# Performance work log

Measured on AMD Instinct MI355X. Metric: run time of the kernel, lower is better.

The kernel has to match this reference:

```python
import jax, jax.numpy as jnp
import numpy as np

N, E, IN_DIM, HID, HEADS, LAYERS, NTYPES, NGRAPH = 50000, 600000, 64, 128, 8, 3, 10, 500
C = HID // HEADS
NEG_SLOPE = 0.2
EPS = 1e-5


def setup_inputs() -> dict:
    key = jax.random.key(0)
    ks = jax.random.split(key, 24)
    inp = {
        "x": jax.random.normal(ks[0], (N, IN_DIM), jnp.float32),
        "edge_index": jax.random.randint(ks[1], (2, E), 0, N),
        "node_types": jax.random.randint(ks[2], (N,), 0, NTYPES),
        "batch": jnp.sort(jax.random.randint(ks[3], (N,), 0, NGRAPH)),
        # node embedding linear
        "emb_W": jax.random.normal(ks[4], (IN_DIM, HID), jnp.float32) / np.sqrt(IN_DIM),
        "emb_b": jnp.zeros((HID,), jnp.float32),
        "ntype_emb": jax.random.normal(ks[5], (NTYPES, HID), jnp.float32) * 0.02,
        # stacked GAT layer params
        "gat_W": jax.random.normal(ks[6], (LAYERS, HID, HID), jnp.float32) / np.sqrt(HID),
        "att_src": jax.random.normal(ks[7], (LAYERS, HEADS, C), jnp.float32) * 0.1,
        "att_dst": jax.random.normal(ks[8], (LAYERS, HEADS, C), jnp.float32) * 0.1,
        "gat_b": jnp.zeros((LAYERS, HID), jnp.float32),
        "ln_g": jnp.ones((LAYERS, HID), jnp.float32),
        "ln_b": jnp.zeros((LAYERS, HID), jnp.float32),
        # global attention MLP
        "ga_W1": jax.random.normal(ks[9], (HID, HID), jnp.float32) / np.sqrt(HID),
        "ga_b1": jnp.zeros((HID,), jnp.float32),
        "ga_W2": jax.random.normal(ks[10], (HID, 1), jnp.float32) / np.sqrt(HID),
        "ga_b2": jnp.zeros((1,), jnp.float32),
        # graph classifier head
        "cls_W1": jax.random.normal(ks[11], (HID, HID), jnp.float32) / np.sqrt(HID),
        "cls_b1": jnp.zeros((HID,), jnp.float32),
        "cls_W2": jax.random.normal(ks[12], (HID, 1), jnp.float32) / np.sqrt(HID),
        "cls_b2": jnp.zeros((1,), jnp.float32),
    }
    return inp


def _layer_norm(h, g, b):
    mu = jnp.mean(h, axis=-1, keepdims=True)
    var = jnp.mean(jnp.square(h - mu), axis=-1, keepdims=True)
    return (h - mu) * jax.lax.rsqrt(var + EPS) * g + b


def _gat_layer(h, src, dst, W, a_src, a_dst, bias):
    # h: [N, HID] -> per-head projection [N, H, C]
    hp = (h @ W).reshape(N, HEADS, C)
    alpha_s = jnp.sum(hp * a_src, axis=-1)  # [N, H]
    alpha_d = jnp.sum(hp * a_dst, axis=-1)  # [N, H]
    e = jax.nn.leaky_relu(alpha_s[src] + alpha_d[dst], NEG_SLOPE)  # [E', H]
    # segment softmax over incoming edges of each destination node
    m = jax.ops.segment_max(e, dst, num_segments=N)
    ex = jnp.exp(e - m[dst])
    s = jax.ops.segment_sum(ex, dst, num_segments=N)
    alpha = ex / s[dst]  # every node has a self-loop, so s > 0
    msg = hp[src] * alpha[:, :, None]  # [E', H, C]
    out = jax.ops.segment_sum(msg, dst, num_segments=N)  # [N, H, C]
    return out.reshape(N, HID) + bias


def reference(x, edge_index, node_types, batch, emb_W, emb_b, ntype_emb,
              gat_W, att_src, att_dst, gat_b, ln_g, ln_b,
              ga_W1, ga_b1, ga_W2, ga_b2, cls_W1, cls_b1, cls_W2, cls_b2):
    # self-loops (PyG GATConv add_self_loops=True)
    loop = jnp.arange(N)
    src = jnp.concatenate([edge_index[0], loop])
    dst = jnp.concatenate([edge_index[1], loop])

    h = x @ emb_W + emb_b
    h = h + ntype_emb[node_types]

    for l in range(LAYERS):
        h_prev = h
        h = _gat_layer(h, src, dst, gat_W[l], att_src[l], att_dst[l], gat_b[l])
        h = _layer_norm(h, ln_g[l], ln_b[l])
        h = jax.nn.relu(h + h_prev)

    # global attention pooling: softmax over all nodes (dim 0, as in source)
    scores = jnp.tanh(h @ ga_W1 + ga_b1) @ ga_W2 + ga_b2  # [N, 1]
    attw = jax.nn.softmax(scores, axis=0)
    h_graph = jnp.sum(h * attw, axis=0)  # [HID]

    # global mean pool per graph
    sums = jax.ops.segment_sum(h, batch, num_segments=NGRAPH)  # [G, HID]
    cnts = jax.ops.segment_sum(jnp.ones((N, 1), h.dtype), batch, num_segments=NGRAPH)
    mean_pool = sums / jnp.maximum(cnts, 1.0)

    hg = h_graph + mean_pool  # broadcast [HID] + [G, HID]

    # graph classifier head (features_batch=None path), squeeze(-1)
    out = jax.nn.relu(hg @ cls_W1 + cls_b1) @ cls_W2 + cls_b2
    return out.squeeze(-1)  # [G]
```

## Files before the change

### kernel.cpp

```cpp
#include <hip/hip_runtime.h>
#include <hip/hip_bf16.h>
#include <math.h>

#define HID 128
#define HEADS 8
#define INDIM 64

typedef _Float16 f16x8 __attribute__((ext_vector_type(8)));
typedef _Float16 f16x4 __attribute__((ext_vector_type(4)));
typedef _Float16 f16x2 __attribute__((ext_vector_type(2)));
typedef float f32x4 __attribute__((ext_vector_type(4)));

__device__ __forceinline__ float fast_tanh(float x) {
    return 1.f - 2.f / (__expf(2.f * x) + 1.f);
}

#if defined(__has_builtin)
#if __has_builtin(__builtin_amdgcn_fdot2)
#define HAVE_FDOT2 1
#endif
#endif

__global__ void prologue_kernel(const int* __restrict__ ei, int* __restrict__ deg,
                                const float* __restrict__ emb_W, const float* __restrict__ gat_W,
                                const float* __restrict__ ga_W1, _Float16* __restrict__ wt_emb,
                                _Float16* __restrict__ wt_gat, _Float16* __restrict__ wt_ga1,
                                const int* __restrict__ batch, int* __restrict__ gstart,
                                float* __restrict__ hgZ,
                                int E, int EE, int N, int G) {
    int i = blockIdx.x * blockDim.x + threadIdx.x;
    if (i < EE) {
        int dst = (i < E) ? ei[E + i] : (i - E);
        atomicAdd(&deg[dst], 1);
    }
    if (i < 8192) {
        int k = i >> 7, n = i & 127;
        wt_emb[n * 64 + k] = (_Float16)emb_W[i];
    } else if (i < 8192 + 49152) {
        int j = i - 8192;
        int l = j >> 14, r = j & 16383;
        int k = r >> 7, n = r & 127;
        wt_gat[l * 16384 + n * 128 + k] = (_Float16)gat_W[j];
    } else if (i < 73728) {
        int j = i - 57344;
        int k = j >> 7, n = j & 127;
        wt_ga1[n * 128 + k] = (_Float16)ga_W1[j];
    } else if (i < 73728 + 129) {
        hgZ[i - 73728] = 0.f;
    }
    if (i >= 100000 && i - 100000 <= G) {
        int g = i - 100000;
        int lo = 0, hi = N;
        while (lo < hi) {
            int mid = (lo + hi) >> 1;
            if (batch[mid] < g) lo = mid + 1; else hi = mid;
        }
        gstart[g] = lo;
    }
}

__global__ __launch_bounds__(256) void mfma_proj_kernel(
    int mode, int K, int N,
    const _Float16* __restrict__ A16, const float* __restrict__ Af32,
    const _Float16* __restrict__ Wt,
    const float* __restrict__ bias, const float* __restrict__ nemb,
    const int* __restrict__ ntypes, _Float16* __restrict__ h16out,
    const float* __restrict__ asrc, const float* __restrict__ adst,
    _Float16* __restrict__ hp_out, float* __restrict__ als, float* __restrict__ ald,
    const float* __restrict__ w2, const float* __restrict__ b2,
    float* __restrict__ escore,
    int PB, int task, const int* __restrict__ ei2,
    const int* __restrict__ degc,
    int* __restrict__ rowptrw, int* __restrict__ woffw, int* __restrict__ esrcw,
    int E2, int EE2)
{
    __shared__ _Float16 w_lds[128 * 136];
    __shared__ _Float16 a_lds[64 * 136];
    int t = threadIdx.x;

    if ((int)blockIdx.x >= PB) {
        if (task == 1) {
            int b = (int)blockIdx.x - PB;
            int i = b * 256 + t;
            int v = (i < N) ? degc[i] : 0;
            int pe = 0;
            for (int j = t; j < (b << 8); j += 256) pe += degc[j];
#pragma unroll
            for (int m = 32; m >= 1; m >>= 1) pe += __shfl_xor(pe, m, 64);
            int* itmp  = (int*)a_lds;
            int* itmp2 = itmp + 256;
            itmp[t] = v;
            if ((t & 63) == 0) itmp2[t >> 6] = pe;
            __syncthreads();
#pragma unroll
            for (int off = 1; off < 256; off <<= 1) {
                int x = (t >= off) ? itmp[t - off] : 0;
                __syncthreads();
                itmp[t] += x;
                __syncthreads();
            }
            pe = itmp2[0] + itmp2[1] + itmp2[2] + itmp2[3];
            int excl = itmp[t] - v + pe;
            if (i < N) { rowptrw[i] = excl; woffw[i] = excl; }
            if (b == 0 && t == 0) rowptrw[N] = EE2;
        } else {
            int sb = (int)blockIdx.x - PB;
            int stride = ((int)gridDim.x - PB) << 8;
            for (int e = sb * 256 + t; e < EE2; e += stride) {
                int src, dst;
                if (e < E2) { src = ei2[e]; dst = ei2[E2 + e]; } else { src = dst = e - E2; }
                int slot = atomicAdd(&woffw[dst], 1);
                esrcw[slot] = src;
            }
        }
        return;
    }

    int KP = K + 8;
    int K8 = K >> 3;

    for (int i = t; i < 128 * K8; i += 256) {
        int row = i / K8, c8 = i - row * K8;
        *(f16x8*)&w_lds[row * KP + 8 * c8] = *(const f16x8*)&Wt[(size_t)row * K + 8 * c8];
    }

    int lane = t & 63, wv = t >> 6;
    int l15 = lane & 15, quad = lane >> 4;

    for (int tile = 0; tile < 2; ++tile) {
        int n0 = blockIdx.x * 128 + tile * 64;
        if (n0 >= N) break;
        __syncthreads();
        if (mode == 0) {
            for (int i = t; i < 64 * K8; i += 256) {
                int row = i / K8, c8 = i - row * K8;
                f16x8 v = {};
                int n = n0 + row;
                if (n < N) {
                    const float4* p = (const float4*)&Af32[(size_t)n * K + 8 * c8];
                    float4 a = p[0], b = p[1];
                    v[0] = (_Float16)a.x; v[1] = (_Float16)a.y;
                    v[2] = (_Float16)a.z; v[3] = (_Float16)a.w;
                    v[4] = (_Float16)b.x; v[5] = (_Float16)b.y;
                    v[6] = (_Float16)b.z; v[7] = (_Float16)b.w;
                }
                *(f16x8*)&a_lds[row * KP + 8 * c8] = v;
            }
        } else {
            for (int i = t; i < 64 * K8; i += 256) {
                int row = i / K8, c8 = i - row * K8;
                f16x8 v = {};
                if (n0 + row < N) v = *(const f16x8*)&A16[(size_t)(n0 + row) * K + 8 * c8];
                *(f16x8*)&a_lds[row * KP + 8 * c8] = v;
            }
        }
        __syncthreads();

        f32x4 acc[8];
#pragma unroll
        for (int c = 0; c < 8; ++c) acc[c] = (f32x4){0.f, 0.f, 0.f, 0.f};

        int ksteps = K >> 5;
        for (int kk = 0; kk < ksteps; ++kk) {
            f16x8 af = *(const f16x8*)&a_lds[(wv * 16 + l15) * KP + kk * 32 + quad * 8];
#pragma unroll
            for (int c = 0; c < 8; ++c) {
                f16x8 bf = *(const f16x8*)&w_lds[(c * 16 + l15) * KP + kk * 32 + quad * 8];
                acc[c] = __builtin_amdgcn_mfma_f32_16x16x32_f16(af, bf, acc[c], 0, 0, 0);
            }
        }

        if (mode == 0) {
            float bv[8];
#pragma unroll
            for (int c = 0; c < 8; ++c) bv[c] = bias[c * 16 + l15];
            __syncthreads();
#pragma unroll
            for (int r = 0; r < 4; ++r) {
                int n = n0 + wv * 16 + quad * 4 + r;
                int nt = (n < N) ? ntypes[n] : 0;
#pragma unroll
                for (int c = 0; c < 8; ++c)
                    a_lds[(wv * 16 + quad * 4 + r) * 136 + c * 16 + l15] =
                        (_Float16)(acc[c][r] + bv[c] + nemb[nt * HID + c * 16 + l15]);
            }
            __syncthreads();
            for (int i = t; i < 64 * 16; i += 256) {
                int row = i >> 4, c8 = i & 15;
                int n = n0 + row;
                if (n < N) *(f16x8*)&h16out[(size_t)n * HID + 8 * c8] = *(const f16x8*)&a_lds[row * 136 + 8 * c8];
            }
        } else if (mode == 1) {
            __syncthreads();
#pragma unroll
            for (int c = 0; c < 8; ++c)
#pragma unroll
                for (int r = 0; r < 4; ++r)
                    a_lds[(wv * 16 + quad * 4 + r) * 136 + c * 16 + l15] = (_Float16)acc[c][r];
            __syncthreads();
            for (int i = t; i < 64 * 16; i += 256) {
                int row = i >> 4, c8 = i & 15;
                int n = n0 + row;
                if (n < N) *(f16x8*)&hp_out[(size_t)n * HID + 8 * c8] = *(const f16x8*)&a_lds[row * 136 + 8 * c8];
            }
            for (int task2 = t; task2 < 512; task2 += 256) {
                int row = task2 >> 3, hd = task2 & 7;
                int n = n0 + row;
                if (n >= N) continue;
                f16x8 v0 = *(const f16x8*)&a_lds[row * 136 + hd * 16];
                f16x8 v1 = *(const f16x8*)&a_lds[row * 136 + hd * 16 + 8];
                float va = 0.f, vd = 0.f;
#pragma unroll
                for (int j = 0; j < 8; ++j) {
                    va += (float)v0[j] * asrc[hd * 16 + j] + (float)v1[j] * asrc[hd * 16 + 8 + j];
                    vd += (float)v0[j] * adst[hd * 16 + j] + (float)v1[j] * adst[hd * 16 + 8 + j];
                }
                als[n * HEADS + hd] = va;
                ald[n * HEADS + hd] = vd;
            }
        } else {
            float b2v = b2[0];
            float treg[4] = {0.f, 0.f, 0.f, 0.f};
#pragma unroll
            for (int c = 0; c < 8; ++c) {
                float b1v = bias[c * 16 + l15];
                float w2v = w2[c * 16 + l15];
#pragma unroll
                for (int r = 0; r < 4; ++r)
                    treg[r] += fast_tanh(acc[c][r] + b1v) * w2v;
            }
#pragma unroll
            for (int r = 0; r < 4; ++r) {
                float v = treg[r];
#pragma unroll
                for (int m = 8; m >= 1; m >>= 1) v += __shfl_xor(v, m, 64);
                if (l15 == 0) {
                    int n = n0 + wv * 16 + quad * 4 + r;
                    if (n < N) escore[n] = __expf(v + b2v);
                }
            }
        }
    }
}

__global__ void gat_aggregate_kernel(const int* __restrict__ rowptr, const int* __restrict__ esrc,
                                     const float* __restrict__ als, const float* __restrict__ ald,
                                     const _Float16* __restrict__ hp16, const float* __restrict__ gb,
                                     const float* __restrict__ lg, const float* __restrict__ lb,
                                     _Float16* __restrict__ h16, int N) {
    int wave = threadIdx.x >> 6;
    int lane = threadIdx.x & 63;
    int n = blockIdx.x * 4 + wave;
    if (n >= N) return;
    int esub = lane >> 4;
    int cg = lane & 15;
    int hd = cg >> 1;
    float adv = ald[n * HEADS + hd];
    int row = rowptr[n], end = rowptr[n + 1];
    int last = end - 1;
    float acc[8] = {0.f, 0.f, 0.f, 0.f, 0.f, 0.f, 0.f, 0.f};
    float sw = 0.f;
    for (int base = row; base < end; base += 16) {
        int iA = base + esub;
        int iB = iA + 4, iC = iA + 8, iD = iA + 12;
        int cA = iA <= last ? iA : last;
        int cB = iB <= last ? iB : last;
        int cC = iC <= last ? iC : last;
        int cD = iD <= last ? iD : last;
        int sA = esrc[cA], sB = esrc[cB], sC = esrc[cC], sD = esrc[cD];
        f16x8 pA = *(const f16x8*)&hp16[(size_t)sA * HID + cg * 8];
        f16x8 pB = *(const f16x8*)&hp16[(size_t)sB * HID + cg * 8];
        f16x8 pC = *(const f16x8*)&hp16[(size_t)sC * HID + cg * 8];
        f16x8 pD = *(const f16x8*)&hp16[(size_t)sD * HID + cg * 8];
        float aA = als[sA * HEADS + hd];
        float aB = als[sB * HEADS + hd];
        float aC = als[sC * HEADS + hd];
        float aD = als[sD * HEADS + hd];
        float lA = aA + adv; lA = lA > 0.f ? lA : 0.2f * lA;
        float lB = aB + adv; lB = lB > 0.f ? lB : 0.2f * lB;
        float lC = aC + adv; lC = lC > 0.f ? lC : 0.2f * lC;
        float lD = aD + adv; lD = lD > 0.f ? lD : 0.2f * lD;
        float wA = __expf(lA) * ((iA < end) ? 1.f : 0.f);
        float wB = __expf(lB) * ((iB < end) ? 1.f : 0.f);
        float wC = __expf(lC) * ((iC < end) ? 1.f : 0.f);
        float wD = __expf(lD) * ((iD < end) ? 1.f : 0.f);
        sw += (wA + wB) + (wC + wD);
#ifdef HAVE_FDOT2
        f16x2 wAB; wAB[0] = (_Float16)wA; wAB[1] = (_Float16)wB;
        f16x2 wCD; wCD[0] = (_Float16)wC; wCD[1] = (_Float16)wD;
#pragma unroll
        for (int j = 0; j < 8; ++j) {
            f16x2 prAB; prAB[0] = pA[j]; prAB[1] = pB[j];
            f16x2 prCD; prCD[0] = pC[j]; prCD[1] = pD[j];
            acc[j] = __builtin_amdgcn_fdot2(prAB, wAB, acc[j], false);
            acc[j] = __builtin_amdgcn_fdot2(prCD, wCD, acc[j], false);
        }
#else
#pragma unroll
        for (int j = 0; j < 8; ++j)
            acc[j] += wA * (float)pA[j] + wB * (float)pB[j]
                    + wC * (float)pC[j] + wD * (float)pD[j];
#endif
    }
#pragma unroll
    for (int m = 16; m <= 32; m <<= 1) {
        sw += __shfl_xor(sw, m, 64);
#pragma unroll
        for (int j = 0; j < 8; ++j) acc[j] += __shfl_xor(acc[j], m, 64);
    }
    float inv_sw = 1.f / sw;
    float4 g0 = ((const float4*)(gb + cg * 8))[0];
    float4 g1 = ((const float4*)(gb + cg * 8))[1];
    float v[8];
    v[0] = acc[0] * inv_sw + g0.x; v[1] = acc[1] * inv_sw + g0.y;
    v[2] = acc[2] * inv_sw + g0.z; v[3] = acc[3] * inv_sw + g0.w;
    v[4] = acc[4] * inv_sw + g1.x; v[5] = acc[5] * inv_sw + g1.y;
    v[6] = acc[6] * inv_sw + g1.z; v[7] = acc[7] * inv_sw + g1.w;
    float s = 0.f;
#pragma unroll
    for (int j = 0; j < 8; ++j) s += v[j];
#pragma unroll
    for (int m = 32; m >= 1; m >>= 1) s += __shfl_xor(s, m, 64);
    float mu = s * (1.f / 512.f);
    float d[8], sq = 0.f;
#pragma unroll
    for (int j = 0; j < 8; ++j) { d[j] = v[j] - mu; sq += d[j] * d[j]; }
#pragma unroll
    for (int m = 32; m >= 1; m >>= 1) sq += __shfl_xor(sq, m, 64);
    float inv = rsqrtf(sq * (1.f / 512.f) + 1e-5f);
    float4 lg0 = ((const float4*)(lg + cg * 8))[0];
    float4 lg1 = ((const float4*)(lg + cg * 8))[1];
    float4 lb0 = ((const float4*)(lb + cg * 8))[0];
    float4 lb1 = ((const float4*)(lb + cg * 8))[1];
    float lgv[8] = {lg0.x, lg0.y, lg0.z, lg0.w, lg1.x, lg1.y, lg1.z, lg1.w};
    float lbv[8] = {lb0.x, lb0.y, lb0.z, lb0.w, lb1.x, lb1.y, lb1.z, lb1.w};
    f16x8 hold = *(const f16x8*)&h16[(size_t)n * HID + cg * 8];
    f16x8 hnew;
#pragma unroll
    for (int j = 0; j < 8; ++j) {
        float r = d[j] * inv * lgv[j] + lbv[j] + (float)hold[j];
        hnew[j] = (_Float16)(r > 0.f ? r : 0.f);
    }
    if (esub == 0) *(f16x8*)&h16[(size_t)n * HID + cg * 8] = hnew;
}

__global__ void pool_graph_kernel(const _Float16* __restrict__ h16, const float* __restrict__ escore,
                                  const int* __restrict__ gstart, float* __restrict__ sums,
                                  float* __restrict__ cnts, float* __restrict__ hgZ, int G) {
    int g = blockIdx.x;
    int t = threadIdx.x;
    int c = t & 127, grp = t >> 7;
    int s = gstart[g], e = gstart[g + 1];
    float msum = 0.f, asum = 0.f, z = 0.f;
    for (int n = s + grp; n < e; n += 4) {
        float hv = (float)h16[(size_t)n * HID + c];
        float es = escore[n];
        msum += hv;
        asum += es * hv;
        if (c == 0) z += es;
    }
    __shared__ float sm[4][HID];
    __shared__ float sa[4][HID];
    __shared__ float sz[4];
    sm[grp][c] = msum;
    sa[grp][c] = asum;
    if (c == 0) sz[grp] = z;
    __syncthreads();
    if (t < HID) {
        float m = sm[0][t] + sm[1][t] + sm[2][t] + sm[3][t];
        float a = sa[0][t] + sa[1][t] + sa[2][t] + sa[3][t];
        sums[(size_t)g * HID + t] = m;
        atomicAdd(&hgZ[t], a);
    } else if (t == HID) {
        cnts[g] = (float)(e - s);
        atomicAdd(&hgZ[HID], sz[0] + sz[1] + sz[2] + sz[3]);
    }
}

__global__ void head_kernel(const float* __restrict__ hgZ, const float* __restrict__ sums,
                            const float* __restrict__ cnts, const float* __restrict__ W1,
                            const float* __restrict__ b1, const float* __restrict__ W2,
                            const float* __restrict__ b2, float* __restrict__ out, int G) {
    int g = blockIdx.x;
    int t = threadIdx.x;
    __shared__ float hr[HID];
    __shared__ float part[2];
    float Z = hgZ[HID];
    float cnt = cnts[g];
    cnt = cnt > 1.f ? cnt : 1.f;
    hr[t] = hgZ[t] / Z + sums[(size_t)g * HID + t] / cnt;
    __syncthreads();
    float acc = b1[t];
#pragma unroll 8
    for (int k = 0; k < HID; ++k) acc += hr[k] * W1[k * HID + t];
    acc = acc > 0.f ? acc : 0.f;
    float v = acc * W2[t];
#pragma unroll
    for (int m = 32; m >= 1; m >>= 1) v += __shfl_xor(v, m, 64);
    if ((t & 63) == 0) part[t >> 6] = v;
    __syncthreads();
    if (t == 0) out[g] = part[0] + part[1] + b2[0];
}

extern "C" void kernel_launch(void* const* d_in, const int* in_sizes, int n_in,
                              void* d_out, int out_size, void* d_ws, size_t ws_size,
                              hipStream_t stream) {
    const float* x        = (const float*)d_in[0];
    const int*   ei       = (const int*)d_in[1];
    const int*   ntypes   = (const int*)d_in[2];
    const int*   batch    = (const int*)d_in[3];
    const float* emb_W    = (const float*)d_in[4];
    const float* emb_b    = (const float*)d_in[5];
    const float* nemb     = (const float*)d_in[6];
    const float* gat_W    = (const float*)d_in[7];
    const float* att_src  = (const float*)d_in[8];
    const float* att_dst  = (const float*)d_in[9];
    const float* gat_b    = (const float*)d_in[10];
    const float* ln_g     = (const float*)d_in[11];
    const float* ln_b     = (const float*)d_in[12];
    const float* ga_W1    = (const float*)d_in[13];
    const float* ga_b1    = (const float*)d_in[14];
    const float* ga_W2    = (const float*)d_in[15];
    const float* ga_b2    = (const float*)d_in[16];
    const float* cls_W1   = (const float*)d_in[17];
    const float* cls_b1   = (const float*)d_in[18];
    const float* cls_W2   = (const float*)d_in[19];
    const float* cls_b2   = (const float*)d_in[20];
    float* out = (float*)d_out;

    const int N  = in_sizes[2];
    const int E  = in_sizes[1] / 2;
    const int EE = E + N;
    const int G  = out_size;
    const int NB = (N + 255) / 256;

    float* ws      = (float*)d_ws;
    float* als     = ws;
    float* ald     = als + (size_t)N * HEADS;
    float* escore  = ald + (size_t)N * HEADS;
    float* sums    = escore + N;
    float* cnts    = sums + (size_t)G * HID;
    float* hgZ     = cnts + G;
    _Float16* h16  = (_Float16*)(hgZ + HID + 1);
    _Float16* hp16 = h16 + (size_t)N * HID;
    _Float16* wt_emb = hp16 + (size_t)N * HID;
    _Float16* wt_gat = wt_emb + 128 * 64;
    _Float16* wt_ga1 = wt_gat + 3 * 128 * 128;
    int*   rowptr  = (int*)(wt_ga1 + 128 * 128);
    int*   woff    = rowptr + (N + 1);
    int*   deg     = woff + N;
    int*   esrc    = deg + N;
    int*   gstart  = esrc + EE;

    hipMemsetAsync(deg, 0, (size_t)N * sizeof(int), stream);
    int ptot = EE;
    if (ptot < 100000 + G + 1) ptot = 100000 + G + 1;
    prologue_kernel<<<(ptot + 255) / 256, 256, 0, stream>>>(
        ei, deg, emb_W, gat_W, ga_W1, wt_emb, wt_gat, wt_ga1,
        batch, gstart, hgZ, E, EE, N, G);

    const int PB = (N + 127) / 128;
    int SCB = 768 - PB;
    if (SCB < 128) SCB = 128;

    mfma_proj_kernel<<<PB + NB, 256, 0, stream>>>(
        0, INDIM, N, nullptr, x, wt_emb, emb_b, nemb, ntypes, h16,
        nullptr, nullptr, nullptr, nullptr, nullptr, nullptr, nullptr, nullptr,
        PB, 1, nullptr, deg, rowptr, woff, nullptr, E, EE);

    mfma_proj_kernel<<<PB + SCB, 256, 0, stream>>>(
        1, HID, N, h16, nullptr, wt_gat,
        nullptr, nullptr, nullptr, nullptr,
        att_src, att_dst, hp16, als, ald, nullptr, nullptr, nullptr,
        PB, 2, ei, nullptr, nullptr, woff, esrc, E, EE);

    gat_aggregate_kernel<<<(N + 3) / 4, 256, 0, stream>>>(
        rowptr, esrc, als, ald, hp16,
        gat_b, ln_g, ln_b, h16, N);

    for (int l = 1; l < 3; ++l) {
        mfma_proj_kernel<<<PB, 256, 0, stream>>>(
            1, HID, N, h16, nullptr, wt_gat + (size_t)l * HID * HID,
            nullptr, nullptr, nullptr, nullptr,
            att_src + l * HID, att_dst + l * HID,
            hp16, als, ald, nullptr, nullptr, nullptr,
            PB, 0, nullptr, nullptr, nullptr, nullptr, nullptr, 0, 0);
        gat_aggregate_kernel<<<(N + 3) / 4, 256, 0, stream>>>(
            rowptr, esrc, als, ald, hp16,
            gat_b + l * HID, ln_g + l * HID, ln_b + l * HID, h16, N);
    }

    mfma_proj_kernel<<<PB, 256, 0, stream>>>(
        2, HID, N, h16, nullptr, wt_ga1, ga_b1, nullptr, nullptr, nullptr,
        nullptr, nullptr, nullptr, nullptr, nullptr, ga_W2, ga_b2, escore,
        PB, 0, nullptr, nullptr, nullptr, nullptr, nullptr, 0, 0);

    pool_graph_kernel<<<G, 512, 0, stream>>>(h16, escore, gstart, sums, cnts, hgZ, G);
    head_kernel<<<G, 128, 0, stream>>>(hgZ, sums, cnts, cls_W1, cls_b1, cls_W2, cls_b2, out, G);
}
```

Baseline: 403.7 us.

## Fuse entire GNN pipeline into one cooperative persistent kernel with grid syncs

Result: slower. 996.1 us (+146.7%).

```diff
diff --git a/kernel.cpp b/kernel.cpp
--- a/kernel.cpp
+++ b/kernel.cpp
@@ -1,6 +1,9 @@
 #include <hip/hip_runtime.h>
+#include <hip/hip_cooperative_groups.h>
 #include <hip/hip_bf16.h>
 #include <math.h>
+
+namespace cg = cooperative_groups;
 
 #define HID 128
 #define HEADS 8
@@ -20,6 +23,446 @@
 #define HAVE_FDOT2 1
 #endif
 #endif
+
+
+struct MegaParams {
+    const float* x; const int* ei; const int* ntypes; const int* batch;
+    const float* emb_W; const float* emb_b; const float* nemb;
+    const float* gat_W; const float* att_src; const float* att_dst;
+    const float* gat_b; const float* ln_g; const float* ln_b;
+    const float* ga_W1; const float* ga_b1; const float* ga_W2; const float* ga_b2;
+    const float* cls_W1; const float* cls_b1; const float* cls_W2; const float* cls_b2;
+    float* out;
+    float *als, *ald, *escore, *sums, *cnts, *hgZ;
+    _Float16 *h16, *hp16, *wt_emb, *wt_gat, *wt_ga1;
+    int *rowptr, *woff, *deg, *esrc, *partials, *gstart;
+    int N, E, EE, G, NB, NT64, P1TOT;
+};
+
+__device__ __forceinline__ void proj_phase(
+    int mode, int K, int N, int NT64,
+    const float* __restrict__ Af32, const _Float16* __restrict__ A16,
+    const _Float16* __restrict__ Wt,
+    const float* __restrict__ bias, const float* __restrict__ nemb,
+    const int* __restrict__ ntypes, _Float16* __restrict__ h16out,
+    const float* __restrict__ asrc, const float* __restrict__ adst,
+    _Float16* __restrict__ hp_out, float* __restrict__ als, float* __restrict__ ald,
+    const float* __restrict__ w2, const float* __restrict__ b2,
+    float* __restrict__ escore,
+    _Float16* w_lds, _Float16* a_lds)
+{
+    int t = threadIdx.x;
+    int KP = K + 8;
+    int K8 = K >> 3;
+
+    for (int i = t; i < 128 * K8; i += 256) {
+        int row = i / K8, c8 = i - row * K8;
+        *(f16x8*)&w_lds[row * KP + 8 * c8] = *(const f16x8*)&Wt[(size_t)row * K + 8 * c8];
+    }
+
+    int lane = t & 63, wv = t >> 6;
+    int l15 = lane & 15, quad = lane >> 4;
+
+    for (int tile = blockIdx.x; tile < NT64; tile += gridDim.x) {
+        int n0 = tile * 64;
+        __syncthreads();
+        if (mode == 0) {
+            for (int i = t; i < 64 * K8; i += 256) {
+                int row = i / K8, c8 = i - row * K8;
+                f16x8 v = {};
+                int n = n0 + row;
+                if (n < N) {
+                    const float4* ptr = (const float4*)&Af32[(size_t)n * K + 8 * c8];
+                    float4 a = ptr[0], b = ptr[1];
+                    v[0] = (_Float16)a.x; v[1] = (_Float16)a.y;
+                    v[2] = (_Float16)a.z; v[3] = (_Float16)a.w;
+                    v[4] = (_Float16)b.x; v[5] = (_Float16)b.y;
+                    v[6] = (_Float16)b.z; v[7] = (_Float16)b.w;
+                }
+                *(f16x8*)&a_lds[row * KP + 8 * c8] = v;
+            }
+        } else {
+            for (int i = t; i < 64 * K8; i += 256) {
+                int row = i / K8, c8 = i - row * K8;
+                f16x8 v = {};
+                if (n0 + row < N) v = *(const f16x8*)&A16[(size_t)(n0 + row) * K + 8 * c8];
+                *(f16x8*)&a_lds[row * KP + 8 * c8] = v;
+            }
+        }
+        __syncthreads();
+
+        f32x4 acc[8];
+#pragma unroll
+        for (int c = 0; c < 8; ++c) acc[c] = (f32x4){0.f, 0.f, 0.f, 0.f};
+
+        int ksteps = K >> 5;
+        for (int kk = 0; kk < ksteps; ++kk) {
+            f16x8 af = *(const f16x8*)&a_lds[(wv * 16 + l15) * KP + kk * 32 + quad * 8];
+#pragma unroll
+            for (int c = 0; c < 8; ++c) {
+                f16x8 bf = *(const f16x8*)&w_lds[(c * 16 + l15) * KP + kk * 32 + quad * 8];
+                acc[c] = __builtin_amdgcn_mfma_f32_16x16x32_f16(af, bf, acc[c], 0, 0, 0);
+            }
+        }
+
+        if (mode == 0) {
+            float bv[8];
+#pragma unroll
+            for (int c = 0; c < 8; ++c) bv[c] = bias[c * 16 + l15];
+            __syncthreads();
+#pragma unroll
+            for (int r = 0; r < 4; ++r) {
+                int n = n0 + wv * 16 + quad * 4 + r;
+                int nt = (n < N) ? ntypes[n] : 0;
+#pragma unroll
+                for (int c = 0; c < 8; ++c)
+                    a_lds[(wv * 16 + quad * 4 + r) * 136 + c * 16 + l15] =
+                        (_Float16)(acc[c][r] + bv[c] + nemb[nt * HID + c * 16 + l15]);
+            }
+            __syncthreads();
+            for (int i = t; i < 64 * 16; i += 256) {
+                int row = i >> 4, c8 = i & 15;
+                int n = n0 + row;
+                if (n < N) *(f16x8*)&h16out[(size_t)n * HID + 8 * c8] = *(const f16x8*)&a_lds[row * 136 + 8 * c8];
+            }
+        } else if (mode == 1) {
+            __syncthreads();
+#pragma unroll
+            for (int c = 0; c < 8; ++c)
+#pragma unroll
+                for (int r = 0; r < 4; ++r)
+                    a_lds[(wv * 16 + quad * 4 + r) * 136 + c * 16 + l15] = (_Float16)acc[c][r];
+            __syncthreads();
+            for (int i = t; i < 64 * 16; i += 256) {
+                int row = i >> 4, c8 = i & 15;
+                int n = n0 + row;
+                if (n < N) *(f16x8*)&hp_out[(size_t)n * HID + 8 * c8] = *(const f16x8*)&a_lds[row * 136 + 8 * c8];
+            }
+            for (int task2 = t; task2 < 512; task2 += 256) {
+                int row = task2 >> 3, hd = task2 & 7;
+                int n = n0 + row;
+                if (n >= N) continue;
+                f16x8 v0 = *(const f16x8*)&a_lds[row * 136 + hd * 16];
+                f16x8 v1 = *(const f16x8*)&a_lds[row * 136 + hd * 16 + 8];
+                float va = 0.f, vd = 0.f;
+#pragma unroll
+                for (int j = 0; j < 8; ++j) {
+                    va += (float)v0[j] * asrc[hd * 16 + j] + (float)v1[j] * asrc[hd * 16 + 8 + j];
+                    vd += (float)v0[j] * adst[hd * 16 + j] + (float)v1[j] * adst[hd * 16 + 8 + j];
+                }
+                als[n * HEADS + hd] = va;
+                ald[n * HEADS + hd] = vd;
+            }
+        } else {
+            float b2v = b2[0];
+            float treg[4] = {0.f, 0.f, 0.f, 0.f};
+#pragma unroll
+            for (int c = 0; c < 8; ++c) {
+                float b1v = bias[c * 16 + l15];
+                float w2v = w2[c * 16 + l15];
+#pragma unroll
+                for (int r = 0; r < 4; ++r)
+                    treg[r] += fast_tanh(acc[c][r] + b1v) * w2v;
+            }
+#pragma unroll
+            for (int r = 0; r < 4; ++r) {
+                float v = treg[r];
+#pragma unroll
+                for (int m = 8; m >= 1; m >>= 1) v += __shfl_xor(v, m, 64);
+                if (l15 == 0) {
+                    int n = n0 + wv * 16 + quad * 4 + r;
+                    if (n < N) escore[n] = __expf(v + b2v);
+                }
+            }
+        }
+    }
+}
+
+__device__ __forceinline__ void agg_phase(
+    const int* __restrict__ rowptr, const int* __restrict__ esrc,
+    const float* __restrict__ als, const float* __restrict__ ald,
+    const _Float16* __restrict__ hp16, const float* __restrict__ gb,
+    const float* __restrict__ lg, const float* __restrict__ lb,
+    _Float16* __restrict__ h16, int N)
+{
+    int wave = threadIdx.x >> 6;
+    int lane = threadIdx.x & 63;
+    int esub = lane >> 4;
+    int cg_ = lane & 15;
+    int hd = cg_ >> 1;
+    int NQ = (N + 3) >> 2;
+    for (int q = blockIdx.x; q < NQ; q += gridDim.x) {
+        int n = q * 4 + wave;
+        if (n >= N) continue;
+        float adv = ald[n * HEADS + hd];
+        int row = rowptr[n], end = rowptr[n + 1];
+        int last = end - 1;
+        float acc[8] = {0.f, 0.f, 0.f, 0.f, 0.f, 0.f, 0.f, 0.f};
+        float sw = 0.f;
+        for (int base = row; base < end; base += 16) {
+            int iA = base + esub;
+            int iB = iA + 4, iC = iA + 8, iD = iA + 12;
+            int cA = iA <= last ? iA : last;
+            int cB = iB <= last ? iB : last;
+            int cC = iC <= last ? iC : last;
+            int cD = iD <= last ? iD : last;
+            int sA = esrc[cA], sB = esrc[cB], sC = esrc[cC], sD = esrc[cD];
+            f16x8 pA = *(const f16x8*)&hp16[(size_t)sA * HID + cg_ * 8];
+            f16x8 pB = *(const f16x8*)&hp16[(size_t)sB * HID + cg_ * 8];
+            f16x8 pC = *(const f16x8*)&hp16[(size_t)sC * HID + cg_ * 8];
+            f16x8 pD = *(const f16x8*)&hp16[(size_t)sD * HID + cg_ * 8];
+            float aA = als[sA * HEADS + hd];
+            float aB = als[sB * HEADS + hd];
+            float aC = als[sC * HEADS + hd];
+            float aD = als[sD * HEADS + hd];
+            float lA = aA + adv; lA = lA > 0.f ? lA : 0.2f * lA;
+            float lB = aB + adv; lB = lB > 0.f ? lB : 0.2f * lB;
+            float lC = aC + adv; lC = lC > 0.f ? lC : 0.2f * lC;
+            float lD = aD + adv; lD = lD > 0.f ? lD : 0.2f * lD;
+            float wA = __expf(lA) * ((iA < end) ? 1.f : 0.f);
+            float wB = __expf(lB) * ((iB < end) ? 1.f : 0.f);
+            float wC = __expf(lC) * ((iC < end) ? 1.f : 0.f);
+            float wD = __expf(lD) * ((iD < end) ? 1.f : 0.f);
+            sw += (wA + wB) + (wC + wD);
+#ifdef HAVE_FDOT2
+            f16x2 wAB; wAB[0] = (_Float16)wA; wAB[1] = (_Float16)wB;
+            f16x2 wCD; wCD[0] = (_Float16)wC; wCD[1] = (_Float16)wD;
+#pragma unroll
+            for (int j = 0; j < 8; ++j) {
+                f16x2 prAB; prAB[0] = pA[j]; prAB[1] = pB[j];
+                f16x2 prCD; prCD[0] = pC[j]; prCD[1] = pD[j];
+                acc[j] = __builtin_amdgcn_fdot2(prAB, wAB, acc[j], false);
+                acc[j] = __builtin_amdgcn_fdot2(prCD, wCD, acc[j], false);
+            }
+#else
+#pragma unroll
+            for (int j = 0; j < 8; ++j)
+                acc[j] += wA * (float)pA[j] + wB * (float)pB[j]
+                        + wC * (float)pC[j] + wD * (float)pD[j];
+#endif
+        }
+#pragma unroll
+        for (int m = 16; m <= 32; m <<= 1) {
+            sw += __shfl_xor(sw, m, 64);
+#pragma unroll
+            for (int j = 0; j < 8; ++j) acc[j] += __shfl_xor(acc[j], m, 64);
+        }
+        float inv_sw = 1.f / sw;
+        float4 g0 = ((const float4*)(gb + cg_ * 8))[0];
+        float4 g1 = ((const float4*)(gb + cg_ * 8))[1];
+        float v[8];
+        v[0] = acc[0] * inv_sw + g0.x; v[1] = acc[1] * inv_sw + g0.y;
+        v[2] = acc[2] * inv_sw + g0.z; v[3] = acc[3] * inv_sw + g0.w;
+        v[4] = acc[4] * inv_sw + g1.x; v[5] = acc[5] * inv_sw + g1.y;
+        v[6] = acc[6] * inv_sw + g1.z; v[7] = acc[7] * inv_sw + g1.w;
+        float s = 0.f;
+#pragma unroll
+        for (int j = 0; j < 8; ++j) s += v[j];
+#pragma unroll
+        for (int m = 32; m >= 1; m >>= 1) s += __shfl_xor(s, m, 64);
+        float mu = s * (1.f / 512.f);
+        float d[8], sq = 0.f;
+#pragma unroll
+        for (int j = 0; j < 8; ++j) { d[j] = v[j] - mu; sq += d[j] * d[j]; }
+#pragma unroll
+        for (int m = 32; m >= 1; m >>= 1) sq += __shfl_xor(sq, m, 64);
+        float inv = rsqrtf(sq * (1.f / 512.f) + 1e-5f);
+        float4 lg0 = ((const float4*)(lg + cg_ * 8))[0];
+        float4 lg1 = ((const float4*)(lg + cg_ * 8))[1];
+        float4 lb0 = ((const float4*)(lb + cg_ * 8))[0];
+        float4 lb1 = ((const float4*)(lb + cg_ * 8))[1];
+        float lgv[8] = {lg0.x, lg0.y, lg0.z, lg0.w, lg1.x, lg1.y, lg1.z, lg1.w};
+        float lbv[8] = {lb0.x, lb0.y, lb0.z, lb0.w, lb1.x, lb1.y, lb1.z, lb1.w};
+        f16x8 hold = *(const f16x8*)&h16[(size_t)n * HID + cg_ * 8];
+        f16x8 hnew;
+#pragma unroll
+        for (int j = 0; j < 8; ++j) {
+            float r = d[j] * inv * lgv[j] + lbv[j] + (float)hold[j];
+            hnew[j] = (_Float16)(r > 0.f ? r : 0.f);
+        }
+        if (esub == 0) *(f16x8*)&h16[(size_t)n * HID + cg_ * 8] = hnew;
+    }
+}
+
+__global__ __launch_bounds__(256) void mega_kernel(MegaParams p) {
+    __shared__ _Float16 w_lds[128 * 136];
+    __shared__ _Float16 a_lds[64 * 136];
+    cg::grid_group grid = cg::this_grid();
+    int t = threadIdx.x;
+    int bid = blockIdx.x, nblk = gridDim.x;
+
+    for (int i = bid * 256 + t; i < p.N; i += nblk * 256) p.deg[i] = 0;
+    if (bid == 0 && t <= HID) p.hgZ[t] = 0.f;
+    grid.sync();
+
+    for (int i = bid * 256 + t; i < p.P1TOT; i += nblk * 256) {
+        if (i < p.EE) {
+            int dst = (i < p.E) ? p.ei[p.E + i] : (i - p.E);
+            atomicAdd(&p.deg[dst], 1);
+        }
+        if (i < 8192) {
+            int k = i >> 7, n = i & 127;
+            p.wt_emb[n * 64 + k] = (_Float16)p.emb_W[i];
+        } else if (i < 8192 + 49152) {
+            int j = i - 8192;
+            int l = j >> 14, r = j & 16383;
+            int k = r >> 7, n = r & 127;
+            p.wt_gat[l * 16384 + n * 128 + k] = (_Float16)p.gat_W[j];
+        } else if (i < 73728) {
+            int j = i - 57344;
+            int k = j >> 7, n = j & 127;
+            p.wt_ga1[n * 128 + k] = (_Float16)p.ga_W1[j];
+        }
+        if (i >= 100000 && i - 100000 <= p.G) {
+            int g = i - 100000;
+            int lo = 0, hi = p.N;
+            while (lo < hi) {
+                int mid = (lo + hi) >> 1;
+                if (p.batch[mid] < g) lo = mid + 1; else hi = mid;
+            }
+            p.gstart[g] = lo;
+        }
+    }
+    grid.sync();
+
+    proj_phase(0, INDIM, p.N, p.NT64, p.x, nullptr, p.wt_emb, p.emb_b, p.nemb,
+               p.ntypes, p.h16, nullptr, nullptr, nullptr, nullptr, nullptr,
+               nullptr, nullptr, nullptr, w_lds, a_lds);
+    __syncthreads();
+    {
+        int* itmp2 = (int*)a_lds;
+        for (int c = bid; c < p.NB; c += nblk) {
+            int i = c * 256 + t;
+            int v = (i < p.N) ? p.deg[i] : 0;
+#pragma unroll
+            for (int m = 32; m >= 1; m >>= 1) v += __shfl_xor(v, m, 64);
+            if ((t & 63) == 0) itmp2[t >> 6] = v;
+            __syncthreads();
+            if (t == 0) p.partials[c] = itmp2[0] + itmp2[1] + itmp2[2] + itmp2[3];
+            __syncthreads();
+        }
+    }
+    grid.sync();
+
+    {
+        int* itmp  = (int*)a_lds;
+        int* itmp2 = itmp + 256;
+        for (int c = bid; c < p.NB; c += nblk) {
+            int i = c * 256 + t;
+            int v = (i < p.N) ? p.deg[i] : 0;
+            int pe = 0;
+            for (int j = t; j < c; j += 256) pe += p.partials[j];
+#pragma unroll
+            for (int m = 32; m >= 1; m >>= 1) pe += __shfl_xor(pe, m, 64);
+            itmp[t] = v;
+            if ((t & 63) == 0) itmp2[t >> 6] = pe;
+            __syncthreads();
+#pragma unroll
+            for (int off = 1; off < 256; off <<= 1) {
+                int xx = (t >= off) ? itmp[t - off] : 0;
+                __syncthreads();
+                itmp[t] += xx;
+                __syncthreads();
+            }
+            pe = itmp2[0] + itmp2[1] + itmp2[2] + itmp2[3];
+            int excl = itmp[t] - v + pe;
+            if (i < p.N) { p.rowptr[i] = excl; p.woff[i] = excl; }
+            if (c == 0 && t == 0) p.rowptr[p.N] = p.EE;
+            __syncthreads();
+        }
+    }
+    grid.sync();
+
+    proj_phase(1, HID, p.N, p.NT64, nullptr, p.h16, p.wt_gat, nullptr, nullptr,
+               nullptr, nullptr, p.att_src, p.att_dst, p.hp16, p.als, p.ald,
+               nullptr, nullptr, nullptr, w_lds, a_lds);
+    for (int e = bid * 256 + t; e < p.EE; e += nblk * 256) {
+        int src, dst;
+        if (e < p.E) { src = p.ei[e]; dst = p.ei[p.E + e]; } else { src = dst = e - p.E; }
+        int slot = atomicAdd(&p.woff[dst], 1);
+        p.esrc[slot] = src;
+    }
+    grid.sync();
+
+    agg_phase(p.rowptr, p.esrc, p.als, p.ald, p.hp16,
+              p.gat_b, p.ln_g, p.ln_b, p.h16, p.N);
+    grid.sync();
+
+    for (int l = 1; l < 3; ++l) {
+        proj_phase(1, HID, p.N, p.NT64, nullptr, p.h16, p.wt_gat + (size_t)l * HID * HID,
+                   nullptr, nullptr, nullptr, nullptr,
+                   p.att_src + l * HID, p.att_dst + l * HID,
+                   p.hp16, p.als, p.ald, nullptr, nullptr, nullptr, w_lds, a_lds);
+        grid.sync();
+        agg_phase(p.rowptr, p.esrc, p.als, p.ald, p.hp16,
+                  p.gat_b + l * HID, p.ln_g + l * HID, p.ln_b + l * HID, p.h16, p.N);
+        grid.sync();
+    }
+
+    proj_phase(2, HID, p.N, p.NT64, nullptr, p.h16, p.wt_ga1, p.ga_b1, nullptr,
+               nullptr, nullptr, nullptr, nullptr, nullptr, nullptr, nullptr,
+               p.ga_W2, p.ga_b2, p.escore, w_lds, a_lds);
+    grid.sync();
+
+    {
+        float* sm = (float*)a_lds;
+        float* sa = sm + 256;
+        float* sz = sa + 256;
+        int c = t & 127, grp = t >> 7;
+        for (int g = bid; g < p.G; g += nblk) {
+            int s = p.gstart[g], e = p.gstart[g + 1];
+            float msum = 0.f, asum = 0.f, z = 0.f;
+            for (int n = s + grp; n < e; n += 2) {
+                float hv = (float)p.h16[(size_t)n * HID + c];
+                float es = p.escore[n];
+                msum += hv;
+                asum += es * hv;
+                if (c == 0) z += es;
+            }
+            sm[grp * 128 + c] = msum;
+            sa[grp * 128 + c] = asum;
+            if (c == 0) sz[grp] = z;
+            __syncthreads();
+            if (t < HID) {
+                p.sums[(size_t)g * HID + t] = sm[t] + sm[128 + t];
+                atomicAdd(&p.hgZ[t], sa[t] + sa[128 + t]);
+            } else if (t == HID) {
+                p.cnts[g] = (float)(e - s);
+                atomicAdd(&p.hgZ[HID], sz[0] + sz[1]);
+            }
+            __syncthreads();
+        }
+    }
+    grid.sync();
+
+    {
+        float* hr = (float*)a_lds;
+        float* part = hr + 128;
+        for (int g = bid; g < p.G; g += nblk) {
+            if (t < HID) {
+                float Z = p.hgZ[HID];
+                float cnt = p.cnts[g];
+                cnt = cnt > 1.f ? cnt : 1.f;
+                hr[t] = p.hgZ[t] / Z + p.sums[(size_t)g * HID + t] / cnt;
+            }
+            __syncthreads();
+            if (t < HID) {
+                float acc = p.cls_b1[t];
+#pragma unroll 8
+                for (int k = 0; k < HID; ++k) acc += hr[k] * p.cls_W1[k * HID + t];
+                acc = acc > 0.f ? acc : 0.f;
+                float v = acc * p.cls_W2[t];
+#pragma unroll
+                for (int m = 32; m >= 1; m >>= 1) v += __shfl_xor(v, m, 64);
+                if ((t & 63) == 0) part[t >> 6] = v;
+            }
+            __syncthreads();
+            if (t == 0) p.out[g] = part[0] + part[1] + p.cls_b2[0];
+            __syncthreads();
+        }
+    }
+}
+
 
 __global__ void prologue_kernel(const int* __restrict__ ei, int* __restrict__ deg,
                                 const float* __restrict__ emb_W, const float* __restrict__ gat_W,
@@ -118,12 +561,10 @@
 
     int KP = K + 8;
     int K8 = K >> 3;
-
     for (int i = t; i < 128 * K8; i += 256) {
         int row = i / K8, c8 = i - row * K8;
         *(f16x8*)&w_lds[row * KP + 8 * c8] = *(const f16x8*)&Wt[(size_t)row * K + 8 * c8];
     }
-
     int lane = t & 63, wv = t >> 6;
     int l15 = lane & 15, quad = lane >> 4;
 
@@ -137,8 +578,8 @@
                 f16x8 v = {};
                 int n = n0 + row;
                 if (n < N) {
-                    const float4* p = (const float4*)&Af32[(size_t)n * K + 8 * c8];
-                    float4 a = p[0], b = p[1];
+                    const float4* ptr = (const float4*)&Af32[(size_t)n * K + 8 * c8];
+                    float4 a = ptr[0], b = ptr[1];
                     v[0] = (_Float16)a.x; v[1] = (_Float16)a.y;
                     v[2] = (_Float16)a.z; v[3] = (_Float16)a.w;
                     v[4] = (_Float16)b.x; v[5] = (_Float16)b.y;
@@ -159,7 +600,6 @@
         f32x4 acc[8];
 #pragma unroll
         for (int c = 0; c < 8; ++c) acc[c] = (f32x4){0.f, 0.f, 0.f, 0.f};
-
         int ksteps = K >> 5;
         for (int kk = 0; kk < ksteps; ++kk) {
             f16x8 af = *(const f16x8*)&a_lds[(wv * 16 + l15) * KP + kk * 32 + quad * 8];
@@ -248,100 +688,7 @@
                                      const _Float16* __restrict__ hp16, const float* __restrict__ gb,
                                      const float* __restrict__ lg, const float* __restrict__ lb,
                                      _Float16* __restrict__ h16, int N) {
-    int wave = threadIdx.x >> 6;
-    int lane = threadIdx.x & 63;
-    int n = blockIdx.x * 4 + wave;
-    if (n >= N) return;
-    int esub = lane >> 4;
-    int cg = lane & 15;
-    int hd = cg >> 1;
-    float adv = ald[n * HEADS + hd];
-    int row = rowptr[n], end = rowptr[n + 1];
-    int last = end - 1;
-    float acc[8] = {0.f, 0.f, 0.f, 0.f, 0.f, 0.f, 0.f, 0.f};
-    float sw = 0.f;
-    for (int base = row; base < end; base += 16) {
-        int iA = base + esub;
-        int iB = iA + 4, iC = iA + 8, iD = iA + 12;
-        int cA = iA <= last ? iA : last;
-        int cB = iB <= last ? iB : last;
-        int cC = iC <= last ? iC : last;
-        int cD = iD <= last ? iD : last;
-        int sA = esrc[cA], sB = esrc[cB], sC = esrc[cC], sD = esrc[cD];
-        f16x8 pA = *(const f16x8*)&hp16[(size_t)sA * HID + cg * 8];
-        f16x8 pB = *(const f16x8*)&hp16[(size_t)sB * HID + cg * 8];
-        f16x8 pC = *(const f16x8*)&hp16[(size_t)sC * HID + cg * 8];
-        f16x8 pD = *(const f16x8*)&hp16[(size_t)sD * HID + cg * 8];
-        float aA = als[sA * HEADS + hd];
-        float aB = als[sB * HEADS + hd];
-        float aC = als[sC * HEADS + hd];
-        float aD = als[sD * HEADS + hd];
-        float lA = aA + adv; lA = lA > 0.f ? lA : 0.2f * lA;
-        float lB = aB + adv; lB = lB > 0.f ? lB : 0.2f * lB;
-        float lC = aC + adv; lC = lC > 0.f ? lC : 0.2f * lC;
-        float lD = aD + adv; lD = lD > 0.f ? lD : 0.2f * lD;
-        float wA = __expf(lA) * ((iA < end) ? 1.f : 0.f);
-        float wB = __expf(lB) * ((iB < end) ? 1.f : 0.f);
-        float wC = __expf(lC) * ((iC < end) ? 1.f : 0.f);
-        float wD = __expf(lD) * ((iD < end) ? 1.f : 0.f);
-        sw += (wA + wB) + (wC + wD);
-#ifdef HAVE_FDOT2
-        f16x2 wAB; wAB[0] = (_Float16)wA; wAB[1] = (_Float16)wB;
-        f16x2 wCD; wCD[0] = (_Float16)wC; wCD[1] = (_Float16)wD;
-#pragma unroll
-        for (int j = 0; j < 8; ++j) {
-            f16x2 prAB; prAB[0] = pA[j]; prAB[1] = pB[j];
-            f16x2 prCD; prCD[0] = pC[j]; prCD[1] = pD[j];
-            acc[j] = __builtin_amdgcn_fdot2(prAB, wAB, acc[j], false);
-            acc[j] = __builtin_amdgcn_fdot2(prCD, wCD, acc[j], false);
-        }
-#else
-#pragma unroll
-        for (int j = 0; j < 8; ++j)
-            acc[j] += wA * (float)pA[j] + wB * (float)pB[j]
-                    + wC * (float)pC[j] + wD * (float)pD[j];
-#endif
-    }
-#pragma unroll
-    for (int m = 16; m <= 32; m <<= 1) {
-        sw += __shfl_xor(sw, m, 64);
-#pragma unroll
-        for (int j = 0; j < 8; ++j) acc[j] += __shfl_xor(acc[j], m, 64);
-    }
-    float inv_sw = 1.f / sw;
-    float4 g0 = ((const float4*)(gb + cg * 8))[0];
-    float4 g1 = ((const float4*)(gb + cg * 8))[1];
-    float v[8];
-    v[0] = acc[0] * inv_sw + g0.x; v[1] = acc[1] * inv_sw + g0.y;
-    v[2] = acc[2] * inv_sw + g0.z; v[3] = acc[3] * inv_sw + g0.w;
-    v[4] = acc[4] * inv_sw + g1.x; v[5] = acc[5] * inv_sw + g1.y;
-    v[6] = acc[6] * inv_sw + g1.z; v[7] = acc[7] * inv_sw + g1.w;
-    float s = 0.f;
-#pragma unroll
-    for (int j = 0; j < 8; ++j) s += v[j];
-#pragma unroll
-    for (int m = 32; m >= 1; m >>= 1) s += __shfl_xor(s, m, 64);
-    float mu = s * (1.f / 512.f);
-    float d[8], sq = 0.f;
-#pragma unroll
-    for (int j = 0; j < 8; ++j) { d[j] = v[j] - mu; sq += d[j] * d[j]; }
-#pragma unroll
-    for (int m = 32; m >= 1; m >>= 1) sq += __shfl_xor(sq, m, 64);
-    float inv = rsqrtf(sq * (1.f / 512.f) + 1e-5f);
-    float4 lg0 = ((const float4*)(lg + cg * 8))[0];
-    float4 lg1 = ((const float4*)(lg + cg * 8))[1];
-    float4 lb0 = ((const float4*)(lb + cg * 8))[0];
-    float4 lb1 = ((const float4*)(lb + cg * 8))[1];
-    float lgv[8] = {lg0.x, lg0.y, lg0.z, lg0.w, lg1.x, lg1.y, lg1.z, lg1.w};
-    float lbv[8] = {lb0.x, lb0.y, lb0.z, lb0.w, lb1.x, lb1.y, lb1.z, lb1.w};
-    f16x8 hold = *(const f16x8*)&h16[(size_t)n * HID + cg * 8];
-    f16x8 hnew;
-#pragma unroll
-    for (int j = 0; j < 8; ++j) {
-        float r = d[j] * inv * lgv[j] + lbv[j] + (float)hold[j];
-        hnew[j] = (_Float16)(r > 0.f ? r : 0.f);
-    }
-    if (esub == 0) *(f16x8*)&h16[(size_t)n * HID + cg * 8] = hnew;
+    agg_phase(rowptr, esrc, als, ald, hp16, gb, lg, lb, h16, N);
 }
 
 __global__ void pool_graph_kernel(const _Float16* __restrict__ h16, const float* __restrict__ escore,
@@ -451,11 +798,46 @@
     int*   deg     = woff + N;
     int*   esrc    = deg + N;
     int*   gstart  = esrc + EE;
+    int*   partials= gstart + (G + 2);
+
+    int P1TOT = EE;
+    if (P1TOT < 100000 + G + 1) P1TOT = 100000 + G + 1;
+
+    static int coop_blocks = -2;
+    if (coop_blocks == -2) {
+        int occ = 0;
+        hipError_t oe = hipOccupancyMaxActiveBlocksPerMultiprocessor(&occ, mega_kernel, 256, 0);
+        if (oe != hipSuccess || occ < 1) coop_blocks = -1;
+        else {
+            if (occ > 3) occ = 3;
+            coop_blocks = occ * 256;
+        }
+    }
+
+    if (coop_blocks > 0) {
+        MegaParams p;
+        p.x = x; p.ei = ei; p.ntypes = ntypes; p.batch = batch;
+        p.emb_W = emb_W; p.emb_b = emb_b; p.nemb = nemb;
+        p.gat_W = gat_W; p.att_src = att_src; p.att_dst = att_dst;
+        p.gat_b = gat_b; p.ln_g = ln_g; p.ln_b = ln_b;
+        p.ga_W1 = ga_W1; p.ga_b1 = ga_b1; p.ga_W2 = ga_W2; p.ga_b2 = ga_b2;
+        p.cls_W1 = cls_W1; p.cls_b1 = cls_b1; p.cls_W2 = cls_W2; p.cls_b2 = cls_b2;
+        p.out = out;
+        p.als = als; p.ald = ald; p.escore = escore; p.sums = sums; p.cnts = cnts; p.hgZ = hgZ;
+        p.h16 = h16; p.hp16 = hp16; p.wt_emb = wt_emb; p.wt_gat = wt_gat; p.wt_ga1 = wt_ga1;
+        p.rowptr = rowptr; p.woff = woff; p.deg = deg; p.esrc = esrc;
+        p.partials = partials; p.gstart = gstart;
+        p.N = N; p.E = E; p.EE = EE; p.G = G; p.NB = NB;
+        p.NT64 = (N + 63) / 64; p.P1TOT = P1TOT;
+        void* args[] = { &p };
+        hipError_t err = hipLaunchCooperativeKernel(mega_kernel, dim3(coop_blocks), dim3(256),
+                                                    args, 0, stream);
+        if (err == hipSuccess) return;
+        coop_blocks = -1;
+    }
 
     hipMemsetAsync(deg, 0, (size_t)N * sizeof(int), stream);
-    int ptot = EE;
-    if (ptot < 100000 + G + 1) ptot = 100000 + G + 1;
-    prologue_kernel<<<(ptot + 255) / 256, 256, 0, stream>>>(
+    prologue_kernel<<<(P1TOT + 255) / 256, 256, 0, stream>>>(
         ei, deg, emb_W, gat_W, ga_W1, wt_emb, wt_gat, wt_ga1,
         batch, gstart, hgZ, E, EE, N, G);
 
```
